# Optimization experiments

Measured on AMD Instinct MI355X. Metric: run time of the kernel, lower is better.

## Reference

```python
import jax, jax.numpy as jnp
import numpy as np

S = 2          # scale_int = ceil(scale)
K = 3          # kernel size
OUTC = 3       # num_out_ch
NUM_FEAT = 64


def conv3x3(x, w, b):
    y = jax.lax.conv_general_dilated(x, w, (1, 1), ((1, 1), (1, 1)),
                                     dimension_numbers=('NCHW', 'OIHW', 'NCHW'))
    return y + b[None, :, None, None]


def unfold3x3(x):
    # torch F.unfold(x, 3, padding=1): (N, C*9, H*W), order c*9 + ki*3 + kj
    N, C, H, W = x.shape
    xp = jnp.pad(x, ((0, 0), (0, 0), (1, 1), (1, 1)))
    patches = jnp.stack([xp[:, :, i:i + H, j:j + W]
                         for i in range(3) for j in range(3)], axis=2)  # (N,C,9,H,W)
    return patches.reshape(N, C * 9, H * W)


def setup_inputs() -> dict:
    key = jax.random.key(0)
    ks = jax.random.split(key, 12)
    b, t, c, h, w = 2, 4, 16, 64, 64
    H, W = S * h, S * w
    nf4 = 64 // 4  # 16
    d_w = K * K * NUM_FEAT * OUTC  # 1728
    return {
        'x0': jax.random.normal(ks[0], (b, NUM_FEAT, h, w), jnp.float32),
        'feature': jax.random.normal(ks[1], (b, t, c, h, w), jnp.float32),
        'pos_mat': jax.random.uniform(ks[2], (H, W, 3), jnp.float32),
        'mask': jnp.ones((b, OUTC, H, W), dtype=bool),
        'conv1_w': jax.random.normal(ks[3], (nf4, 64, 3, 3), jnp.float32) * 0.05,
        'conv1_b': jnp.zeros((nf4,), jnp.float32),
        'conv2_w': jax.random.normal(ks[4], (nf4, nf4, 3, 3), jnp.float32) * 0.05,
        'conv2_b': jnp.zeros((nf4,), jnp.float32),
        'f2w1_w': jax.random.normal(ks[5], (256, nf4 + 1), jnp.float32) * 0.05,
        'f2w1_b': jnp.zeros((256,), jnp.float32),
        'f2w2_w': jax.random.normal(ks[6], (d_w, 256), jnp.float32) * 0.05,
        'f2w2_b': jnp.zeros((d_w,), jnp.float32),
    }


def reference(x0, feature, pos_mat, mask, conv1_w, conv1_b, conv2_w, conv2_b,
              f2w1_w, f2w1_b, f2w2_w, f2w2_b):
    b, t, c, h, w = feature.shape
    H, W = S * h, S * w
    # with_gradBack=False -> feature.detach()
    feat = jax.lax.stop_gradient(feature).reshape(b, t * c, h, w)
    # repeat_x(..., upsample=True): nearest-neighbour upsample by S
    feat_up = jnp.repeat(jnp.repeat(feat, S, axis=2), S, axis=3)  # (b,64,H,W)
    f = jax.nn.relu(conv3x3(feat_up, conv1_w, conv1_b))
    f = conv3x3(f, conv2_w, conv2_b)                              # (b,16,H,W)
    pos0 = jnp.transpose(pos_mat, (2, 0, 1))[0:1]                 # (1,H,W)
    fm = jnp.concatenate([f, jnp.broadcast_to(pos0[None], (b, 1, H, W))], axis=1)
    fm = fm.reshape(b, -1, H * W).transpose(0, 2, 1)              # (b,HW,17)
    hdn = jax.nn.relu(fm @ f2w1_w.T + f2w1_b)
    weights = hdn @ f2w2_w.T + f2w2_b                             # (b,HW,1728)
    weights = weights.reshape(b, h, S, w, S, K * K * NUM_FEAT, OUTC)
    weights = jnp.transpose(weights, (0, 2, 4, 1, 3, 5, 6))
    weights = weights.reshape(b, S * S, h * w, K * K * NUM_FEAT, OUTC)
    # repeat_x(x0) tiles x0 S^2 times -> all S^2 col copies identical; compute once
    cols = unfold3x3(x0).transpose(0, 2, 1)                       # (b,hw,576)
    out = jnp.einsum('bpk,bspko->bspo', cols, weights)            # (b,S^2,hw,3)
    out = jnp.transpose(out, (0, 1, 3, 2)).reshape(b, S, S, OUTC, h, w)
    out = jnp.transpose(out, (0, 3, 4, 1, 5, 2)).reshape(b, OUTC, H, W)
    # integer scale -> mask all True -> masked_select + view is identity
    return out, weights
```

## Files before the change

kernel.cpp:

```cpp
#include <hip/hip_runtime.h>

#define THREADS 256

#define Bsz 2
#define HWp 16384
#define Ntot (Bsz*HWp)
#define HID 256
#define Mm 1728
#define FMC 17
#define W_OFF 98304

#define F1_OFF  0
#define F1_SZ   (Bsz*16*HWp)
#define WB2_OFF (F1_SZ + Ntot*FMC)
#define WB1_OFF (WB2_OFF + (Mm*HID)/2)

typedef __attribute__((ext_vector_type(8))) short bf16x8;
typedef __attribute__((ext_vector_type(4))) float f32x4;

static __device__ __forceinline__ short f2bf(float x) {
    unsigned u = __builtin_bit_cast(unsigned, x);
    unsigned r = (u + 0x7fff + ((u >> 16) & 1)) >> 16;
    return (short)r;
}
static __device__ __forceinline__ float bf2f(short s) {
    unsigned u = ((unsigned)(unsigned short)s) << 16;
    return __builtin_bit_cast(float, u);
}

__global__ __launch_bounds__(THREADS) void k13_conv1_cvt(const float* __restrict__ feat,
                                                         const float* __restrict__ w1,
                                                         const float* __restrict__ b1,
                                                         float* __restrict__ f1,
                                                         const float* __restrict__ w2g,
                                                         short* __restrict__ wB2,
                                                         const float* __restrict__ w1g,
                                                         short* __restrict__ wB1) {
    int tid = threadIdx.x;
    if (blockIdx.x >= 944) {
        for (int idx = tid; idx < 8192; idx += THREADS) {
            int i = idx & 7, l = (idx >> 3) & 63, h = idx >> 9;
            int k = (l >> 4) * 8 + i, hid = h * 16 + (l & 15);
            wB1[idx] = (k < FMC) ? f2bf(w1g[hid * FMC + k]) : (short)0;
        }
        return;
    }
    if (blockIdx.x >= 512) {
        int t4 = ((blockIdx.x - 512) * THREADS + tid) * 4;
        int i = t4 & 7, l = (t4 >> 3) & 63, ct = (t4 >> 9) & 3, s = (t4 >> 11) & 7, mc = t4 >> 14;
        int col = mc * 64 + ct * 16 + (l & 15);
        int k0 = s * 32 + (l >> 4) * 8 + i;
        f32x4 w = *(const f32x4*)(w2g + col * HID + k0);
        short4 o;
        o.x = f2bf(w[0]); o.y = f2bf(w[1]); o.z = f2bf(w[2]); o.w = f2bf(w[3]);
        *(short4*)(wB2 + t4) = o;
        return;
    }
    __shared__ float sW[4 * 64 * 4];
    int b = blockIdx.x;
    int rg = b & 15, oc = (b >> 4) & 15, bb = b >> 8;
    int c = tid & 63, r = rg * 4 + (tid >> 6);

    #pragma unroll
    for (int q = 0; q < 4; ++q) {
        int e = tid * 4 + q;
        int v = e & 1, u = (e >> 1) & 1, ic = (e >> 2) & 63, pp = (e >> 8) & 3;
        int pi = pp >> 1, pj = pp & 1;
        float s = 0.f;
        for (int ki = 0; ki < 3; ++ki) {
            bool okki = pi ? (u ? (ki == 2) : (ki <= 1)) : (u ? (ki >= 1) : (ki == 0));
            if (!okki) continue;
            for (int kj = 0; kj < 3; ++kj) {
                bool okkj = pj ? (v ? (kj == 2) : (kj <= 1)) : (v ? (kj >= 1) : (kj == 0));
                if (okkj) s += w1[((oc * 64 + ic) * 3 + ki) * 3 + kj];
            }
        }
        sW[(pp * 64 + ic) * 4 + u * 2 + v] = s;
    }
    __syncthreads();

    float bias = b1[oc];
    float a00 = bias, a01 = bias, a10 = bias, a11 = bias;

    float mt = (r > 0) ? 1.f : 0.f, mb2 = (r < 63) ? 1.f : 0.f;
    float ml = (c > 0) ? 1.f : 0.f, mr2 = (c < 63) ? 1.f : 0.f;
    int ro0 = (r > 0) ? -64 : 0, ro2 = (r < 63) ? 64 : 0;
    int co0 = (c > 0) ? -1 : 0, co2 = (c < 63) ? 1 : 0;

    const float* fb = feat + bb * 64 * 4096 + r * 64 + c;
    for (int ic = 0; ic < 64; ++ic) {
        const float* p1 = fb + ic * 4096;
        const float* p0 = p1 + ro0;
        const float* p2 = p1 + ro2;
        float v00 = p0[co0] * (mt * ml), v01 = p0[0] * mt, v02 = p0[co2] * (mt * mr2);
        float v10 = p1[co0] * ml,        v11 = p1[0],      v12 = p1[co2] * mr2;
        float v20 = p2[co0] * (mb2 * ml), v21 = p2[0] * mb2, v22 = p2[co2] * (mb2 * mr2);

        f32x4 w0 = *(const f32x4*)(sW + (0 * 64 + ic) * 4);
        f32x4 w1v = *(const f32x4*)(sW + (1 * 64 + ic) * 4);
        f32x4 w2v = *(const f32x4*)(sW + (2 * 64 + ic) * 4);
        f32x4 w3 = *(const f32x4*)(sW + (3 * 64 + ic) * 4);

        a00 = fmaf(w0[0], v00, a00); a00 = fmaf(w0[1], v01, a00);
        a00 = fmaf(w0[2], v10, a00); a00 = fmaf(w0[3], v11, a00);
        a01 = fmaf(w1v[0], v01, a01); a01 = fmaf(w1v[1], v02, a01);
        a01 = fmaf(w1v[2], v11, a01); a01 = fmaf(w1v[3], v12, a01);
        a10 = fmaf(w2v[0], v10, a10); a10 = fmaf(w2v[1], v11, a10);
        a10 = fmaf(w2v[2], v20, a10); a10 = fmaf(w2v[3], v21, a10);
        a11 = fmaf(w3[0], v11, a11); a11 = fmaf(w3[1], v12, a11);
        a11 = fmaf(w3[2], v21, a11); a11 = fmaf(w3[3], v22, a11);
    }

    float* fo = f1 + (bb * 16 + oc) * HWp + (2 * r) * 128 + 2 * c;
    *reinterpret_cast<float2*>(fo)       = make_float2(fmaxf(a00, 0.f), fmaxf(a01, 0.f));
    *reinterpret_cast<float2*>(fo + 128) = make_float2(fmaxf(a10, 0.f), fmaxf(a11, 0.f));
}

__global__ __launch_bounds__(THREADS, 3) void k4_fused(const float* __restrict__ f1,
                                                       const float* __restrict__ w2,
                                                       const float* __restrict__ b2,
                                                       const float* __restrict__ pos,
                                                       const short* __restrict__ wB1,
                                                       const float* __restrict__ b1g,
                                                       const short* __restrict__ wB2,
                                                       const float* __restrict__ b2g,
                                                       const float* __restrict__ x0g,
                                                       float* __restrict__ dout) {
    __shared__ short sA[16384];
    __shared__ int   sOB[64];
    __shared__ float uni[4084];

    short* sF  = (short*)uni;
    float* sFM = uni + 1584;
    short* sXT = (short*)uni;
    float* sOut = uni + 3316;

    int tid = threadIdx.x;
    int n0 = blockIdx.x * 64;
    int bb = n0 >> 14, tt = n0 & 16383, I = tt >> 7, J0 = tt & 127;
    int i0 = I >> 1, jmin = J0 >> 1;

    for (int e = tid; e < 3168; e += THREADS) {
        int jc = e % 66, r2 = e / 66;
        int di = r2 % 3, ic = r2 / 3;
        int y = I + di - 1, x = J0 + jc - 1;
        float v = 0.f;
        if ((unsigned)y < 128u && (unsigned)x < 128u)
            v = f1[(bb * 16 + ic) * HWp + y * 128 + x];
        sF[(ic * 3 + di) * 66 + jc] = f2bf(v);
    }
    for (int e = tid; e < 2112; e += THREADS) sFM[e] = 0.f;
    if (tid < 64) {
        int J = J0 + tid;
        int s = ((I & 1) << 1) | (J & 1);
        int p = ((I >> 1) << 6) | (J >> 1);
        sOB[tid] = W_OFF + ((bb * 4 + s) * 4096 + p) * Mm;
    }
    __syncthreads();

    {
        int pix = tid & 63, q = tid >> 6;
        float acc[4];
        #pragma unroll
        for (int o = 0; o < 4; ++o) acc[o] = b2[q * 4 + o];
        #pragma unroll 4
        for (int ic = 0; ic < 16; ++ic) {
            float v[9];
            #pragma unroll
            for (int di = 0; di < 3; ++di) {
                const short* row = sF + (ic * 3 + di) * 66 + pix;
                v[di * 3 + 0] = bf2f(row[0]);
                v[di * 3 + 1] = bf2f(row[1]);
                v[di * 3 + 2] = bf2f(row[2]);
            }
            #pragma unroll
            for (int o = 0; o < 4; ++o) {
                const float* w = w2 + ((q * 4 + o) * 16 + ic) * 9;
                acc[o] = fmaf(v[0], w[0], acc[o]); acc[o] = fmaf(v[1], w[1], acc[o]);
                acc[o] = fmaf(v[2], w[2], acc[o]); acc[o] = fmaf(v[3], w[3], acc[o]);
                acc[o] = fmaf(v[4], w[4], acc[o]); acc[o] = fmaf(v[5], w[5], acc[o]);
                acc[o] = fmaf(v[6], w[6], acc[o]); acc[o] = fmaf(v[7], w[7], acc[o]);
                acc[o] = fmaf(v[8], w[8], acc[o]);
            }
        }
        #pragma unroll
        for (int o = 0; o < 4; ++o) sFM[pix * 33 + q * 4 + o] = acc[o];
        if (q == 0) sFM[pix * 33 + 16] = pos[(I * 128 + J0 + pix) * 3];
    }
    __syncthreads();

    int wv = tid >> 6, l = tid & 63, lm = l & 15, lg = l >> 4;

    int row = wv * 16 + lm;
    bf16x8 af1;
    #pragma unroll
    for (int i = 0; i < 8; ++i) af1[i] = f2bf(sFM[row * 33 + lg * 8 + i]);
    __syncthreads();

    {
        const short* wb = wB1 + l * 8;
        int pbase = ((lg >> 1) * 64 + row) * 8 + (lg & 1) * 4;
        #pragma unroll 4
        for (int h = 0; h < 16; ++h) {
            bf16x8 bfr = *(const bf16x8*)(wb + h * 512);
            f32x4 bias = *(const f32x4*)(b1g + h * 16 + lg * 4);
            f32x4 acc = __builtin_amdgcn_mfma_f32_16x16x32_bf16(bfr, af1, bias, 0, 0, 0);
            unsigned c0 = (unsigned short)f2bf(fmaxf(acc[0], 0.f));
            unsigned c1 = (unsigned short)f2bf(fmaxf(acc[1], 0.f));
            unsigned c2 = (unsigned short)f2bf(fmaxf(acc[2], 0.f));
            unsigned c3 = (unsigned short)f2bf(fmaxf(acc[3], 0.f));
            uint2 uv; uv.x = c0 | (c1 << 16); uv.y = c2 | (c3 << 16);
            *(uint2*)(sA + pbase + h * 1024) = uv;
        }
    }
    {
        const float* x0b = x0g + bb * 64 * 4096;
        for (int e = tid; e < 6528; e += THREADS) {
            int ch = e / 102, r2 = e - ch * 102;
            int ki = r2 / 34, jc = r2 - ki * 34;
            int y = i0 + ki - 1, x = jmin + jc - 1;
            float v = 0.f;
            if ((unsigned)y < 64u && (unsigned)x < 64u) v = x0b[(ch * 64 + y) * 64 + x];
            sXT[jc * 195 + ch * 3 + ki] = f2bf(v);
        }
    }
    __syncthreads();

    int lg3 = lg % 3, lg4 = lg * 4;
    int pixbase[4], jl195[4];
    #pragma unroll
    for (int rt = 0; rt < 4; ++rt) {
        pixbase[rt] = sOB[rt * 16 + lm];
        jl195[rt] = (rt * 8 + (lm >> 1)) * 195;
    }

    const short* aptr = sA + lg * 512 + lm * 8;

    float racc[4][3];
    #pragma unroll
    for (int rt = 0; rt < 4; ++rt) {
        racc[rt][0] = 0.f; racc[rt][1] = 0.f; racc[rt][2] = 0.f;
    }

    for (int mc = wv; mc < 27; mc += 4) {
        int m0 = mc * 64;
        f32x4 acc[4][4];
        #pragma unroll
        for (int ct = 0; ct < 4; ++ct) {
            f32x4 bias4 = *(const f32x4*)(b2g + m0 + ct * 16 + lg * 4);
            #pragma unroll
            for (int rt = 0; rt < 4; ++rt)
                acc[rt][ct] = bias4;
        }
        const short* bbase = wB2 + (size_t)mc * 16384 + l * 8;
        #pragma unroll 2
        for (int s = 0; s < 8; ++s) {
            bf16x8 af[4], bfr[4];
            #pragma unroll
            for (int rt = 0; rt < 4; ++rt)
                af[rt] = *(const bf16x8*)(aptr + s * 2048 + rt * 128);
            #pragma unroll
            for (int ct = 0; ct < 4; ++ct)
                bfr[ct] = *(const bf16x8*)(bbase + (s * 4 + ct) * 512);
            #pragma unroll
            for (int rt = 0; rt < 4; ++rt)
                #pragma unroll
                for (int ct = 0; ct < 4; ++ct)
                    acc[rt][ct] = __builtin_amdgcn_mfma_f32_16x16x32_bf16(
                        bfr[ct], af[rt], acc[rt][ct], 0, 0, 0);
        }
        #pragma unroll
        for (int rt = 0; rt < 4; ++rt)
            #pragma unroll
            for (int ct = 0; ct < 4; ++ct)
                *(f32x4*)(dout + pixbase[rt] + m0 + ct * 16 + lg * 4) = acc[rt][ct];
#define ACCUM(QB)                                                              \
        _Pragma("unroll")                                                      \
        for (int ct = 0; ct < 4; ++ct) {                                       \
            int t = m0 + ct * 16 + lg4;                                        \
            int K0 = (t * 21846) >> 16;                                        \
            int rem3 = t - 3 * K0;                                             \
            int Q2 = (K0 * 21846) >> 16;                                       \
            int kja = K0 - 3 * Q2;                                             \
            int kqa = kja * 195 + Q2;                                          \
            int kqb = (kja == 2) ? (Q2 + 1) : (kqa + 195);                     \
            _Pragma("unroll")                                                  \
            for (int rt = 0; rt < 4; ++rt) {                                   \
                float xa = bf2f(sXT[jl195[rt] + kqa]);                         \
                float xb = bf2f(sXT[jl195[rt] + kqb]);                         \
                float x1 = (rem3 == 2) ? xb : xa;                              \
                float x2 = (rem3 >= 1) ? xb : xa;                              \
                racc[rt][(QB + ct) % 3] =                                      \
                    fmaf(acc[rt][ct][0], xa, racc[rt][(QB + ct) % 3]);         \
                racc[rt][(QB + ct + 1) % 3] =                                  \
                    fmaf(acc[rt][ct][1], x1, racc[rt][(QB + ct + 1) % 3]);     \
                racc[rt][(QB + ct + 2) % 3] =                                  \
                    fmaf(acc[rt][ct][2], x2, racc[rt][(QB + ct + 2) % 3]);     \
                racc[rt][(QB + ct) % 3] =                                      \
                    fmaf(acc[rt][ct][3], xb, racc[rt][(QB + ct) % 3]);         \
            }                                                                  \
        }
        switch (mc % 3) {
            case 0: ACCUM(0); break;
            case 1: ACCUM(1); break;
            default: ACCUM(2); break;
        }
#undef ACCUM
    }

    #pragma unroll
    for (int rt = 0; rt < 4; ++rt) {
        float q0 = racc[rt][0], q1 = racc[rt][1], q2 = racc[rt][2];
        float a0 = (lg3 == 0) ? q0 : ((lg3 == 1) ? q2 : q1);
        float a1 = (lg3 == 0) ? q1 : ((lg3 == 1) ? q0 : q2);
        float a2 = (lg3 == 0) ? q2 : ((lg3 == 1) ? q1 : q0);
        a0 += __shfl_xor(a0, 16, 64); a0 += __shfl_xor(a0, 32, 64);
        a1 += __shfl_xor(a1, 16, 64); a1 += __shfl_xor(a1, 32, 64);
        a2 += __shfl_xor(a2, 16, 64); a2 += __shfl_xor(a2, 32, 64);
        if (l < 16) {
            float* so = sOut + (wv * 64 + rt * 16 + lm) * 3;
            so[0] = a0; so[1] = a1; so[2] = a2;
        }
    }
    __syncthreads();
    if (tid < 192) {
        float s = sOut[tid] + sOut[192 + tid] + sOut[384 + tid] + sOut[576 + tid];
        int pix = tid / 3, o = tid - 3 * pix;
        dout[bb * 3 * HWp + o * HWp + I * 128 + J0 + pix] = s;
    }
}

extern "C" void kernel_launch(void* const* d_in, const int* in_sizes, int n_in,
                              void* d_out, int out_size, void* d_ws, size_t ws_size,
                              hipStream_t stream) {
    const float* x0      = (const float*)d_in[0];
    const float* feature = (const float*)d_in[1];
    const float* pos     = (const float*)d_in[2];
    const float* w1      = (const float*)d_in[4];
    const float* b1      = (const float*)d_in[5];
    const float* w2      = (const float*)d_in[6];
    const float* b2      = (const float*)d_in[7];
    const float* f2w1_w  = (const float*)d_in[8];
    const float* f2w1_b  = (const float*)d_in[9];
    const float* f2w2_w  = (const float*)d_in[10];
    const float* f2w2_b  = (const float*)d_in[11];

    float* out = (float*)d_out;
    float* ws  = (float*)d_ws;
    float* f1  = ws + F1_OFF;
    short* wB2 = (short*)(ws + WB2_OFF);
    short* wB1 = (short*)(ws + WB1_OFF);

    k13_conv1_cvt<<<945, THREADS, 0, stream>>>(feature, w1, b1, f1, f2w2_w, wB2,
                                               f2w1_w, wB1);
    k4_fused<<<Ntot / 64, THREADS, 0, stream>>>(f1, w2, b2, pos, wB1, f2w1_b,
                                                wB2, f2w2_b, x0, out);
}
```

Measured before the change: 108.5 us.

## Halve pixel tile per block to 32 and raise occupancy bound to four

The fused conv2+MLP+apply kernel now handles 32 pixels per block instead of 64. That halves shared memory and the MFMA accumulator registers, and the launch bound goes from 3 to 4 waves per SIMD. Each wave now does 2 row tiles instead of 4 in the big GEMM, and the hidden-layer MFMA work is split across waves by hidden chunk. The intent is higher occupancy and more blocks, but each block's wB2 weight fragment loads are reused across only half as many pixels, so weight traffic from L2 per pixel doubles.

```diff
diff --git a/kernel.cpp b/kernel.cpp
--- a/kernel.cpp
+++ b/kernel.cpp
@@ -116,7 +116,7 @@
     *reinterpret_cast<float2*>(fo + 128) = make_float2(fmaxf(a10, 0.f), fmaxf(a11, 0.f));
 }
 
-__global__ __launch_bounds__(THREADS, 3) void k4_fused(const float* __restrict__ f1,
+__global__ __launch_bounds__(THREADS, 4) void k4_fused(const float* __restrict__ f1,
                                                        const float* __restrict__ w2,
                                                        const float* __restrict__ b2,
                                                        const float* __restrict__ pos,
@@ -126,31 +126,31 @@
                                                        const float* __restrict__ b2g,
                                                        const float* __restrict__ x0g,
                                                        float* __restrict__ dout) {
-    __shared__ short sA[16384];
-    __shared__ int   sOB[64];
-    __shared__ float uni[4084];
-
-    short* sF  = (short*)uni;
-    float* sFM = uni + 1584;
-    short* sXT = (short*)uni;
-    float* sOut = uni + 3316;
+    __shared__ short sA[8192];
+    __shared__ int   sOB[32];
+    __shared__ float uni[2144];
+
+    short* sF   = (short*)uni;
+    float* sFM  = uni + 816;
+    short* sXT  = (short*)uni;
+    float* sOut = uni + 1756;
 
     int tid = threadIdx.x;
-    int n0 = blockIdx.x * 64;
+    int n0 = blockIdx.x * 32;
     int bb = n0 >> 14, tt = n0 & 16383, I = tt >> 7, J0 = tt & 127;
     int i0 = I >> 1, jmin = J0 >> 1;
 
-    for (int e = tid; e < 3168; e += THREADS) {
-        int jc = e % 66, r2 = e / 66;
+    for (int e = tid; e < 1632; e += THREADS) {
+        int jc = e % 34, r2 = e / 34;
         int di = r2 % 3, ic = r2 / 3;
         int y = I + di - 1, x = J0 + jc - 1;
         float v = 0.f;
         if ((unsigned)y < 128u && (unsigned)x < 128u)
             v = f1[(bb * 16 + ic) * HWp + y * 128 + x];
-        sF[(ic * 3 + di) * 66 + jc] = f2bf(v);
-    }
-    for (int e = tid; e < 2112; e += THREADS) sFM[e] = 0.f;
-    if (tid < 64) {
+        sF[(ic * 3 + di) * 34 + jc] = f2bf(v);
+    }
+    for (int e = tid; e < 1056; e += THREADS) sFM[e] = 0.f;
+    if (tid < 32) {
         int J = J0 + tid;
         int s = ((I & 1) << 1) | (J & 1);
         int p = ((I >> 1) << 6) | (J >> 1);
@@ -159,121 +159,124 @@
     __syncthreads();
 
     {
-        int pix = tid & 63, q = tid >> 6;
-        float acc[4];
-        #pragma unroll
-        for (int o = 0; o < 4; ++o) acc[o] = b2[q * 4 + o];
+        int pix = tid & 31, q = tid >> 5;
+        float a0 = b2[q * 2], a1 = b2[q * 2 + 1];
         #pragma unroll 4
         for (int ic = 0; ic < 16; ++ic) {
             float v[9];
             #pragma unroll
             for (int di = 0; di < 3; ++di) {
-                const short* row = sF + (ic * 3 + di) * 66 + pix;
+                const short* row = sF + (ic * 3 + di) * 34 + pix;
                 v[di * 3 + 0] = bf2f(row[0]);
                 v[di * 3 + 1] = bf2f(row[1]);
                 v[di * 3 + 2] = bf2f(row[2]);
             }
-            #pragma unroll
-            for (int o = 0; o < 4; ++o) {
-                const float* w = w2 + ((q * 4 + o) * 16 + ic) * 9;
-                acc[o] = fmaf(v[0], w[0], acc[o]); acc[o] = fmaf(v[1], w[1], acc[o]);
-                acc[o] = fmaf(v[2], w[2], acc[o]); acc[o] = fmaf(v[3], w[3], acc[o]);
-                acc[o] = fmaf(v[4], w[4], acc[o]); acc[o] = fmaf(v[5], w[5], acc[o]);
-                acc[o] = fmaf(v[6], w[6], acc[o]); acc[o] = fmaf(v[7], w[7], acc[o]);
-                acc[o] = fmaf(v[8], w[8], acc[o]);
+            const float* w0 = w2 + ((q * 2) * 16 + ic) * 9;
+            const float* w1p = w2 + ((q * 2 + 1) * 16 + ic) * 9;
+            #pragma unroll
+            for (int e = 0; e < 9; ++e) {
+                a0 = fmaf(v[e], w0[e], a0);
+                a1 = fmaf(v[e], w1p[e], a1);
             }
         }
+        sFM[pix * 33 + q * 2]     = a0;
+        sFM[pix * 33 + q * 2 + 1] = a1;
+        if (q == 0) sFM[pix * 33 + 16] = pos[(I * 128 + J0 + pix) * 3];
+    }
+    __syncthreads();
+
+    int wv = tid >> 6, l = tid & 63, lm = l & 15, lg = l >> 4;
+
+    bf16x8 afA, afB;
+    #pragma unroll
+    for (int i = 0; i < 8; ++i) {
+        afA[i] = f2bf(sFM[lm * 33 + lg * 8 + i]);
+        afB[i] = f2bf(sFM[(16 + lm) * 33 + lg * 8 + i]);
+    }
+    __syncthreads();
+
+    {
+        int pbase = ((lg >> 1) * 32 + lm) * 8 + (lg & 1) * 4;
         #pragma unroll
-        for (int o = 0; o < 4; ++o) sFM[pix * 33 + q * 4 + o] = acc[o];
-        if (q == 0) sFM[pix * 33 + 16] = pos[(I * 128 + J0 + pix) * 3];
-    }
-    __syncthreads();
-
-    int wv = tid >> 6, l = tid & 63, lm = l & 15, lg = l >> 4;
-
-    int row = wv * 16 + lm;
-    bf16x8 af1;
-    #pragma unroll
-    for (int i = 0; i < 8; ++i) af1[i] = f2bf(sFM[row * 33 + lg * 8 + i]);
-    __syncthreads();
-
-    {
-        const short* wb = wB1 + l * 8;
-        int pbase = ((lg >> 1) * 64 + row) * 8 + (lg & 1) * 4;
-        #pragma unroll 4
-        for (int h = 0; h < 16; ++h) {
-            bf16x8 bfr = *(const bf16x8*)(wb + h * 512);
+        for (int hh = 0; hh < 4; ++hh) {
+            int h = wv * 4 + hh;
+            bf16x8 bfr = *(const bf16x8*)(wB1 + l * 8 + h * 512);
             f32x4 bias = *(const f32x4*)(b1g + h * 16 + lg * 4);
-            f32x4 acc = __builtin_amdgcn_mfma_f32_16x16x32_bf16(bfr, af1, bias, 0, 0, 0);
-            unsigned c0 = (unsigned short)f2bf(fmaxf(acc[0], 0.f));
-            unsigned c1 = (unsigned short)f2bf(fmaxf(acc[1], 0.f));
-            unsigned c2 = (unsigned short)f2bf(fmaxf(acc[2], 0.f));
-            unsigned c3 = (unsigned short)f2bf(fmaxf(acc[3], 0.f));
-            uint2 uv; uv.x = c0 | (c1 << 16); uv.y = c2 | (c3 << 16);
-            *(uint2*)(sA + pbase + h * 1024) = uv;
+            f32x4 accA = __builtin_amdgcn_mfma_f32_16x16x32_bf16(bfr, afA, bias, 0, 0, 0);
+            f32x4 accB = __builtin_amdgcn_mfma_f32_16x16x32_bf16(bfr, afB, bias, 0, 0, 0);
+            unsigned a0 = (unsigned short)f2bf(fmaxf(accA[0], 0.f));
+            unsigned a1 = (unsigned short)f2bf(fmaxf(accA[1], 0.f));
+            unsigned a2 = (unsigned short)f2bf(fmaxf(accA[2], 0.f));
+            unsigned a3 = (unsigned short)f2bf(fmaxf(accA[3], 0.f));
+            uint2 uvA; uvA.x = a0 | (a1 << 16); uvA.y = a2 | (a3 << 16);
+            *(uint2*)(sA + pbase + h * 512) = uvA;
+            unsigned b0 = (unsigned short)f2bf(fmaxf(accB[0], 0.f));
+            unsigned b1_ = (unsigned short)f2bf(fmaxf(accB[1], 0.f));
+            unsigned b2_ = (unsigned short)f2bf(fmaxf(accB[2], 0.f));
+            unsigned b3 = (unsigned short)f2bf(fmaxf(accB[3], 0.f));
+            uint2 uvB; uvB.x = b0 | (b1_ << 16); uvB.y = b2_ | (b3 << 16);
+            *(uint2*)(sA + pbase + 128 + h * 512) = uvB;
         }
     }
     {
         const float* x0b = x0g + bb * 64 * 4096;
-        for (int e = tid; e < 6528; e += THREADS) {
-            int ch = e / 102, r2 = e - ch * 102;
-            int ki = r2 / 34, jc = r2 - ki * 34;
+        for (int e = tid; e < 3456; e += THREADS) {
+            int jc = e / 192, q = e - jc * 192;
+            int ch = q / 3, ki = q - ch * 3;
             int y = i0 + ki - 1, x = jmin + jc - 1;
             float v = 0.f;
             if ((unsigned)y < 64u && (unsigned)x < 64u) v = x0b[(ch * 64 + y) * 64 + x];
-            sXT[jc * 195 + ch * 3 + ki] = f2bf(v);
+            sXT[jc * 195 + q] = f2bf(v);
         }
     }
     __syncthreads();
 
     int lg3 = lg % 3, lg4 = lg * 4;
-    int pixbase[4], jl195[4];
-    #pragma unroll
-    for (int rt = 0; rt < 4; ++rt) {
+    int pixbase[2], jl195[2];
+    #pragma unroll
+    for (int rt = 0; rt < 2; ++rt) {
         pixbase[rt] = sOB[rt * 16 + lm];
         jl195[rt] = (rt * 8 + (lm >> 1)) * 195;
     }
 
-    const short* aptr = sA + lg * 512 + lm * 8;
-
-    float racc[4][3];
-    #pragma unroll
-    for (int rt = 0; rt < 4; ++rt) {
+    const short* aptr = sA + lg * 256 + lm * 8;
+
+    float racc[2][3];
+    #pragma unroll
+    for (int rt = 0; rt < 2; ++rt) {
         racc[rt][0] = 0.f; racc[rt][1] = 0.f; racc[rt][2] = 0.f;
     }
 
     for (int mc = wv; mc < 27; mc += 4) {
         int m0 = mc * 64;
-        f32x4 acc[4][4];
+        f32x4 acc[2][4];
         #pragma unroll
         for (int ct = 0; ct < 4; ++ct) {
-            f32x4 bias4 = *(const f32x4*)(b2g + m0 + ct * 16 + lg * 4);
-            #pragma unroll
-            for (int rt = 0; rt < 4; ++rt)
-                acc[rt][ct] = bias4;
+            f32x4 bias4 = *(const f32x4*)(b2g + m0 + ct * 16 + lg4);
+            acc[0][ct] = bias4;
+            acc[1][ct] = bias4;
         }
         const short* bbase = wB2 + (size_t)mc * 16384 + l * 8;
         #pragma unroll 2
         for (int s = 0; s < 8; ++s) {
-            bf16x8 af[4], bfr[4];
-            #pragma unroll
-            for (int rt = 0; rt < 4; ++rt)
-                af[rt] = *(const bf16x8*)(aptr + s * 2048 + rt * 128);
+            bf16x8 af[2], bfr[4];
+            af[0] = *(const bf16x8*)(aptr + s * 1024);
+            af[1] = *(const bf16x8*)(aptr + s * 1024 + 128);
             #pragma unroll
             for (int ct = 0; ct < 4; ++ct)
                 bfr[ct] = *(const bf16x8*)(bbase + (s * 4 + ct) * 512);
             #pragma unroll
-            for (int rt = 0; rt < 4; ++rt)
+            for (int rt = 0; rt < 2; ++rt)
                 #pragma unroll
                 for (int ct = 0; ct < 4; ++ct)
                     acc[rt][ct] = __builtin_amdgcn_mfma_f32_16x16x32_bf16(
                         bfr[ct], af[rt], acc[rt][ct], 0, 0, 0);
         }
         #pragma unroll
-        for (int rt = 0; rt < 4; ++rt)
+        for (int rt = 0; rt < 2; ++rt)
             #pragma unroll
             for (int ct = 0; ct < 4; ++ct)
-                *(f32x4*)(dout + pixbase[rt] + m0 + ct * 16 + lg * 4) = acc[rt][ct];
+                *(f32x4*)(dout + pixbase[rt] + m0 + ct * 16 + lg4) = acc[rt][ct];
 #define ACCUM(QB)                                                              \
         _Pragma("unroll")                                                      \
         for (int ct = 0; ct < 4; ++ct) {                                       \
@@ -285,7 +288,7 @@
             int kqa = kja * 195 + Q2;                                          \
             int kqb = (kja == 2) ? (Q2 + 1) : (kqa + 195);                     \
             _Pragma("unroll")                                                  \
-            for (int rt = 0; rt < 4; ++rt) {                                   \
+            for (int rt = 0; rt < 2; ++rt) {                                   \
                 float xa = bf2f(sXT[jl195[rt] + kqa]);                         \
                 float xb = bf2f(sXT[jl195[rt] + kqb]);                         \
                 float x1 = (rem3 == 2) ? xb : xa;                              \
@@ -309,7 +312,7 @@
     }
 
     #pragma unroll
-    for (int rt = 0; rt < 4; ++rt) {
+    for (int rt = 0; rt < 2; ++rt) {
         float q0 = racc[rt][0], q1 = racc[rt][1], q2 = racc[rt][2];
         float a0 = (lg3 == 0) ? q0 : ((lg3 == 1) ? q2 : q1);
         float a1 = (lg3 == 0) ? q1 : ((lg3 == 1) ? q0 : q2);
@@ -318,13 +321,13 @@
         a1 += __shfl_xor(a1, 16, 64); a1 += __shfl_xor(a1, 32, 64);
         a2 += __shfl_xor(a2, 16, 64); a2 += __shfl_xor(a2, 32, 64);
         if (l < 16) {
-            float* so = sOut + (wv * 64 + rt * 16 + lm) * 3;
+            float* so = sOut + (wv * 32 + rt * 16 + lm) * 3;
             so[0] = a0; so[1] = a1; so[2] = a2;
         }
     }
     __syncthreads();
-    if (tid < 192) {
-        float s = sOut[tid] + sOut[192 + tid] + sOut[384 + tid] + sOut[576 + tid];
+    if (tid < 96) {
+        float s = sOut[tid] + sOut[96 + tid] + sOut[192 + tid] + sOut[288 + tid];
         int pix = tid / 3, o = tid - 3 * pix;
         dout[bb * 3 * HWp + o * HWp + I * 128 + J0 + pix] = s;
     }
@@ -353,6 +356,6 @@
 
     k13_conv1_cvt<<<945, THREADS, 0, stream>>>(feature, w1, b1, f1, f2w2_w, wB2,
                                                f2w1_w, wB1);
-    k4_fused<<<Ntot / 64, THREADS, 0, stream>>>(f1, w2, b2, pos, wB1, f2w1_b,
+    k4_fused<<<Ntot / 32, THREADS, 0, stream>>>(f1, w2, b2, pos, wB1, f2w1_b,
                                                 wB2, f2w2_b, x0, out);
 }
```

Result: slower. 111.3 us (+2.6%).

## Stage weight tile through swizzled LDS for coalesced stores, contiguous per-wave chunk ranges

Applied to the files above, without the earlier changes.

The output tile of each MFMA chunk is first converted to bf16 and written into a per-wave XOR-swizzled LDS staging buffer. It is then read back row-wise so each wave writes contiguous 256-byte segments of the weights output, instead of scattered 16-byte pieces. Waves now take contiguous ranges of the 27 chunks (7/7/7/6) rather than striding. Occupancy drops from 3 to 2 blocks because the extra 32KB LDS stage is needed. The stored weights are rounded to bf16 precision before the float write, which adds error to the output.

```diff
diff --git a/kernel.cpp b/kernel.cpp
--- a/kernel.cpp
+++ b/kernel.cpp
@@ -116,7 +116,7 @@
     *reinterpret_cast<float2*>(fo + 128) = make_float2(fmaxf(a10, 0.f), fmaxf(a11, 0.f));
 }
 
-__global__ __launch_bounds__(THREADS, 3) void k4_fused(const float* __restrict__ f1,
+__global__ __launch_bounds__(THREADS, 2) void k4_fused(const float* __restrict__ f1,
                                                        const float* __restrict__ w2,
                                                        const float* __restrict__ b2,
                                                        const float* __restrict__ pos,
@@ -128,12 +128,12 @@
                                                        float* __restrict__ dout) {
     __shared__ short sA[16384];
     __shared__ int   sOB[64];
-    __shared__ float uni[4084];
+    __shared__ float uni[3696];
+    __shared__ short sStage[16384];
 
     short* sF  = (short*)uni;
     float* sFM = uni + 1584;
     short* sXT = (short*)uni;
-    float* sOut = uni + 3316;
 
     int tid = threadIdx.x;
     int n0 = blockIdx.x * 64;
@@ -227,14 +227,17 @@
     __syncthreads();
 
     int lg3 = lg % 3, lg4 = lg * 4;
-    int pixbase[4], jl195[4];
-    #pragma unroll
-    for (int rt = 0; rt < 4; ++rt) {
-        pixbase[rt] = sOB[rt * 16 + lm];
+    int jl195[4];
+    #pragma unroll
+    for (int rt = 0; rt < 4; ++rt)
         jl195[rt] = (rt * 8 + (lm >> 1)) * 195;
-    }
+
+    int sOBr[16];
+    #pragma unroll
+    for (int g = 0; g < 16; ++g) sOBr[g] = sOB[g * 4 + lg];
 
     const short* aptr = sA + lg * 512 + lm * 8;
+    short* myStage = sStage + wv * 4096;
 
     float racc[4][3];
     #pragma unroll
@@ -242,38 +245,6 @@
         racc[rt][0] = 0.f; racc[rt][1] = 0.f; racc[rt][2] = 0.f;
     }
 
-    for (int mc = wv; mc < 27; mc += 4) {
-        int m0 = mc * 64;
-        f32x4 acc[4][4];
-        #pragma unroll
-        for (int ct = 0; ct < 4; ++ct) {
-            f32x4 bias4 = *(const f32x4*)(b2g + m0 + ct * 16 + lg * 4);
-            #pragma unroll
-            for (int rt = 0; rt < 4; ++rt)
-                acc[rt][ct] = bias4;
-        }
-        const short* bbase = wB2 + (size_t)mc * 16384 + l * 8;
-        #pragma unroll 2
-        for (int s = 0; s < 8; ++s) {
-            bf16x8 af[4], bfr[4];
-            #pragma unroll
-            for (int rt = 0; rt < 4; ++rt)
-                af[rt] = *(const bf16x8*)(aptr + s * 2048 + rt * 128);
-            #pragma unroll
-            for (int ct = 0; ct < 4; ++ct)
-                bfr[ct] = *(const bf16x8*)(bbase + (s * 4 + ct) * 512);
-            #pragma unroll
-            for (int rt = 0; rt < 4; ++rt)
-                #pragma unroll
-                for (int ct = 0; ct < 4; ++ct)
-                    acc[rt][ct] = __builtin_amdgcn_mfma_f32_16x16x32_bf16(
-                        bfr[ct], af[rt], acc[rt][ct], 0, 0, 0);
-        }
-        #pragma unroll
-        for (int rt = 0; rt < 4; ++rt)
-            #pragma unroll
-            for (int ct = 0; ct < 4; ++ct)
-                *(f32x4*)(dout + pixbase[rt] + m0 + ct * 16 + lg * 4) = acc[rt][ct];
 #define ACCUM(QB)                                                              \
         _Pragma("unroll")                                                      \
         for (int ct = 0; ct < 4; ++ct) {                                       \
@@ -300,13 +271,70 @@
                     fmaf(acc[rt][ct][3], xb, racc[rt][(QB + ct) % 3]);         \
             }                                                                  \
         }
+
+    int lo = (wv < 3) ? wv * 7 : 21;
+    int hi = (wv < 3) ? (lo + 7) : 27;
+    for (int mc = lo; mc < hi; ++mc) {
+        int m0 = mc * 64;
+        f32x4 acc[4][4];
+        #pragma unroll
+        for (int ct = 0; ct < 4; ++ct) {
+            f32x4 bias4 = *(const f32x4*)(b2g + m0 + ct * 16 + lg4);
+            #pragma unroll
+            for (int rt = 0; rt < 4; ++rt)
+                acc[rt][ct] = bias4;
+        }
+        const short* bbase = wB2 + (size_t)mc * 16384 + l * 8;
+        #pragma unroll 2
+        for (int s = 0; s < 8; ++s) {
+            bf16x8 af[4], bfr[4];
+            #pragma unroll
+            for (int rt = 0; rt < 4; ++rt)
+                af[rt] = *(const bf16x8*)(aptr + s * 2048 + rt * 128);
+            #pragma unroll
+            for (int ct = 0; ct < 4; ++ct)
+                bfr[ct] = *(const bf16x8*)(bbase + (s * 4 + ct) * 512);
+            #pragma unroll
+            for (int rt = 0; rt < 4; ++rt)
+                #pragma unroll
+                for (int ct = 0; ct < 4; ++ct)
+                    acc[rt][ct] = __builtin_amdgcn_mfma_f32_16x16x32_bf16(
+                        bfr[ct], af[rt], acc[rt][ct], 0, 0, 0);
+        }
+        #pragma unroll
+        for (int rt = 0; rt < 4; ++rt) {
+            int pxb = (rt * 16 + lm) * 64;
+            #pragma unroll
+            for (int ct = 0; ct < 4; ++ct) {
+                int up = (((ct * 4 + lg) ^ lm) << 2);
+                short4 sv;
+                sv.x = f2bf(acc[rt][ct][0]); sv.y = f2bf(acc[rt][ct][1]);
+                sv.z = f2bf(acc[rt][ct][2]); sv.w = f2bf(acc[rt][ct][3]);
+                *(short4*)(myStage + pxb + up) = sv;
+            }
+        }
         switch (mc % 3) {
             case 0: ACCUM(0); break;
             case 1: ACCUM(1); break;
             default: ACCUM(2); break;
         }
+        #pragma unroll
+        for (int g = 0; g < 16; ++g) {
+            int px = g * 4 + lg;
+            int up = ((lm ^ (px & 15)) << 2);
+            uint2 uv = *(const uint2*)(myStage + px * 64 + up);
+            f32x4 v;
+            v[0] = __builtin_bit_cast(float, uv.x << 16);
+            v[1] = __builtin_bit_cast(float, uv.x & 0xffff0000u);
+            v[2] = __builtin_bit_cast(float, uv.y << 16);
+            v[3] = __builtin_bit_cast(float, uv.y & 0xffff0000u);
+            *(f32x4*)(dout + sOBr[g] + m0 + lm * 4) = v;
+        }
+    }
 #undef ACCUM
-    }
+
+    __syncthreads();
+    float* sOut = (float*)sStage;
 
     #pragma unroll
     for (int rt = 0; rt < 4; ++rt) {
```

Result: faster. 106.3 us (median of 2 runs) (-2.1%).
